# Kernel tuning notes

Measured on AMD Instinct MI355X. Metric: run time of the kernel, lower is better.

The kernel has to match this reference:

```python
import math
import jax, jax.numpy as jnp
import numpy as np

B, T, D_MODEL, H = 8, 2048, 1024, 16
D_HEAD = D_MODEL // H


def _rel_shift(x):
    # x: (B, T, H, H) -- faithful port of the TF pad/reshape/slice trick,
    # which in this module operates on the time axis (dim 1).
    b, t, h, h2 = x.shape
    x = jnp.pad(x, ((0, 0), (1, 0), (0, 0), (0, 0)))  # (B, T+1, H, H)
    x = x.reshape(t + 1, b, h, h2)[1:]                 # drop first row
    return x.reshape(b, t, h, h2)


def setup_inputs() -> dict:
    key = jax.random.key(0)
    ks = jax.random.split(key, 16)
    s = 1.0 / math.sqrt(D_MODEL)
    return {
        "inputs": jax.random.normal(ks[0], (B, T, D_MODEL), jnp.float32),
        "pos_embedding": jax.random.normal(ks[1], (B, T, D_MODEL), jnp.float32),
        "masks": jnp.ones((B, T), dtype=bool),
        "Wq": jax.random.normal(ks[2], (D_MODEL, D_MODEL), jnp.float32) * s,
        "bq": jnp.zeros((D_MODEL,), jnp.float32),
        "Wk": jax.random.normal(ks[3], (D_MODEL, D_MODEL), jnp.float32) * s,
        "bk": jnp.zeros((D_MODEL,), jnp.float32),
        "Wv": jax.random.normal(ks[4], (D_MODEL, D_MODEL), jnp.float32) * s,
        "bv": jnp.zeros((D_MODEL,), jnp.float32),
        "Wp": jax.random.normal(ks[5], (D_MODEL, D_MODEL), jnp.float32) * s,
        "Wo": jax.random.normal(ks[6], (D_MODEL, D_MODEL), jnp.float32) * s,
        "bo": jnp.zeros((D_MODEL,), jnp.float32),
        "u_bias": jax.random.normal(ks[7], (H, D_HEAD), jnp.float32) * 0.05,
        "v_bias": jax.random.normal(ks[8], (H, D_HEAD), jnp.float32) * 0.05,
    }


def reference(inputs, pos_embedding, masks, Wq, bq, Wk, bk, Wv, bv, Wp, Wo, bo, u_bias, v_bias):
    b, t, _ = inputs.shape
    sqrt_dim = math.sqrt(D_MODEL)
    q = (inputs @ Wq + bq).reshape(b, t, H, D_HEAD)
    k = (inputs @ Wk + bk).reshape(b, t, H, D_HEAD)
    v = (inputs @ Wv + bv).reshape(b, t, H, D_HEAD)
    p = (pos_embedding @ Wp).reshape(b, t, H, D_HEAD)

    # NOTE: no (B,H,T,D) transpose in the original -> HxH scores per timestep.
    content_score = jnp.einsum("bthd,btkd->bthk", q + u_bias, k)  # (B,T,H,H)
    pos_score = jnp.einsum("bthd,btkd->bthk", q + v_bias, p)      # (B,T,H,H)
    pos_score = _rel_shift(pos_score)
    score = (content_score + pos_score) / sqrt_dim
    score = jnp.where(masks[:, :, None, None], score, jnp.float32(1e-9))
    attn = jax.nn.softmax(score, axis=-1)
    ctx = jnp.einsum("bthk,btkd->bthd", attn, v)                  # (B,T,H,D)
    ctx = ctx.transpose(0, 2, 1, 3).reshape(b, -1, D_MODEL)       # (B,T,d_model)
    return ctx @ Wo + bo
```

## Files before the change

kernel.cpp:

```cpp
#include <hip/hip_runtime.h>


typedef __attribute__((ext_vector_type(8))) short short8;
typedef __attribute__((ext_vector_type(4))) float f32x4;

__device__ __forceinline__ ushort f2bf(float f) {
    unsigned u = __float_as_uint(f);
    u += 0x7FFFu + ((u >> 16) & 1u);
    return (ushort)(u >> 16);
}
__device__ __forceinline__ float bf2f(ushort u) {
    return __uint_as_float(((unsigned)u) << 16);
}

typedef const unsigned int __attribute__((address_space(1)))* gas_t;
typedef unsigned int __attribute__((address_space(3)))* las_t;
__device__ __forceinline__ void gl_lds16(const ushort* g, ushort* l) {
    __builtin_amdgcn_global_load_lds((gas_t)g, (las_t)l, 16, 0, 0);
}

__global__ __launch_bounds__(256)
void conv_bf16_k(const float* __restrict__ in, ushort* __restrict__ out)
{
    const size_t i = ((size_t)blockIdx.x * 256 + threadIdx.x) * 8;
    float4 a = *(const float4*)(in + i);
    float4 b = *(const float4*)(in + i + 4);
    short8 o = {(short)f2bf(a.x), (short)f2bf(a.y), (short)f2bf(a.z), (short)f2bf(a.w),
                (short)f2bf(b.x), (short)f2bf(b.y), (short)f2bf(b.z), (short)f2bf(b.w)};
    *(short8*)(out + i) = o;
}

__global__ __launch_bounds__(256)
void transpose5_k(const float* __restrict__ W0, const float* __restrict__ W1,
                  const float* __restrict__ W2, const float* __restrict__ W3,
                  const float* __restrict__ W4, ushort* __restrict__ Wt)
{
    __shared__ float tile[32][33];
    const int z = blockIdx.z;
    const float* W = (z == 0) ? W0 : (z == 1) ? W1 : (z == 2) ? W2 : (z == 3) ? W3 : W4;
    ushort* dst = Wt + (size_t)z * 1024 * 1024;
    const int tx = threadIdx.x & 31;
    const int ty = threadIdx.x >> 5;
    const int n0 = blockIdx.x * 32;
    const int k0 = blockIdx.y * 32;
#pragma unroll
    for (int i = 0; i < 4; ++i)
        tile[ty + i * 8][tx] = W[(size_t)(k0 + ty + i * 8) * 1024 + n0 + tx];
    __syncthreads();
#pragma unroll
    for (int i = 0; i < 4; ++i)
        dst[(size_t)(n0 + ty + i * 8) * 1024 + k0 + tx] = f2bf(tile[tx][ty + i * 8]);
}

__global__ __launch_bounds__(256)
void bias_concat_k(const float* __restrict__ b0, const float* __restrict__ b1,
                   const float* __restrict__ b2, float* __restrict__ out)
{
    const int i = blockIdx.x * 256 + threadIdx.x;
    const int s = i >> 10;
    const int j = i & 1023;
    out[i] = (s == 0) ? b0[j] : (s == 1) ? b1[j] : b2[j];
}


#define VMC(n) asm volatile("s_waitcnt vmcnt(" #n ")" ::: "memory")
#define KDIM 1024

template<int HAS_BIAS, int OUT_BF16>
__global__ __launch_bounds__(512, 4)
void gemm7_k(const ushort* __restrict__ A, const ushort* __restrict__ Bt,
             const float* __restrict__ bias, void* __restrict__ Cv,
             int N)
{
    __shared__ ushort As[3 * 4096];
    __shared__ ushort Bs[3 * 8192];
    const int tid = threadIdx.x;
    const int l = tid & 63;
    const int w = tid >> 6;
    const int wr = w >> 2;
    const int wc = w & 3;

    const int gx = gridDim.x;
    const int lin = blockIdx.y * gx + blockIdx.x;
    const int xcd = lin & 7;
    const int idx = lin >> 3;
    const int hb = gridDim.y >> 3;
    const int sxc = gx >> 2;
    const int g4 = idx >> 4;
    const int li = idx & 15;
    const int bx = (g4 % sxc) * 4 + (li & 3);
    const int by = xcd * hb + (g4 / sxc) * 4 + (li >> 2);
    const int bm = by * 128;
    const int bn = bx * 256;

    const int srow = tid >> 2;
    const int scol = ((tid & 3) ^ ((tid >> 3) & 3)) * 8;
    const ushort* Ag  = A  + (size_t)(bm + srow) * KDIM + scol;
    const ushort* Bg  = Bt + (size_t)(bn + srow) * KDIM + scol;
    const ushort* Bg2 = Bg + (size_t)128 * KDIM;
    const int lw = w * 512;

    const int lr = l & 15;
    const int fb = (((l >> 4) ^ ((l >> 1) & 3)) * 8);
    const int laneA = (wr * 64 + lr) * 32 + fb;
    const int laneB = (wc * 64 + lr) * 32 + fb;

    f32x4 acc[4][4];
#pragma unroll
    for (int i = 0; i < 4; ++i)
#pragma unroll
        for (int n = 0; n < 4; ++n)
            acc[i][n] = (f32x4){0.f, 0.f, 0.f, 0.f};

#define STAGE7(tt, rg) do { \
    ushort* ha = As + (rg) * 4096 + lw; \
    ushort* hbp = Bs + (rg) * 8192 + lw; \
    const size_t ko = (size_t)(tt) * 32; \
    gl_lds16(Ag + ko, ha); \
    gl_lds16(Bg + ko, hbp); \
    gl_lds16(Bg2 + ko, hbp + 4096); \
} while (0)

    STAGE7(0, 0);
    STAGE7(1, 1);
    VMC(3);
    __builtin_amdgcn_s_barrier();
    __builtin_amdgcn_sched_barrier(0);

#pragma unroll
    for (int t = 0; t < 32; ++t) {
        const int cur = t % 3;
        const int stg = (t + 2) % 3;
        if (t + 2 < 32) STAGE7(t + 2, stg);
        const ushort* ap = As + cur * 4096 + laneA;
        const ushort* bp = Bs + cur * 8192 + laneB;
        short8 af[4], bf4[4];
#pragma unroll
        for (int m = 0; m < 4; ++m) af[m] = *(const short8*)(ap + m * 512);
#pragma unroll
        for (int n = 0; n < 4; ++n) bf4[n] = *(const short8*)(bp + n * 512);
        if (t < 30) { VMC(3); }
        else if (t == 30) { VMC(0); }
        asm volatile("s_waitcnt lgkmcnt(0)" ::: "memory");
        __builtin_amdgcn_s_barrier();
        __builtin_amdgcn_sched_barrier(0);
#pragma unroll
        for (int m = 0; m < 4; ++m)
#pragma unroll
            for (int n = 0; n < 4; ++n)
                acc[m][n] = __builtin_amdgcn_mfma_f32_16x16x32_bf16(af[m], bf4[n], acc[m][n], 0, 0, 0);
    }
#undef STAGE7

    const int cr = (l >> 4) * 4;
    const int cc = l & 15;
    float bv[4];
#pragma unroll
    for (int n = 0; n < 4; ++n)
        bv[n] = HAS_BIAS ? bias[bn + wc * 64 + n * 16 + cc] : 0.f;
#pragma unroll
    for (int m = 0; m < 4; ++m) {
#pragma unroll
        for (int n = 0; n < 4; ++n) {
            const int col = bn + wc * 64 + n * 16 + cc;
#pragma unroll
            for (int r = 0; r < 4; ++r) {
                const int row = bm + wr * 64 + m * 16 + cr + r;
                float v = acc[m][n][r] + bv[n];
                if (OUT_BF16) ((ushort*)Cv)[(size_t)row * N + col] = f2bf(v);
                else          ((float*)Cv)[(size_t)row * N + col] = v;
            }
        }
    }
}

__global__ __launch_bounds__(256)
void attn2_k(const ushort* __restrict__ qkv, const ushort* __restrict__ pbuf,
             const float* __restrict__ ubias, const float* __restrict__ vbias,
             const int* __restrict__ masks, ushort* __restrict__ ctx)
{
    __shared__ __align__(16) float Pl[4][16 * 20];

    const int tid = threadIdx.x;
    const int w = tid >> 6;
    const int l = tid & 63;
    const int m = blockIdx.x * 4 + w;
    const int b2 = m >> 11;
    const int t2 = m & 2047;
    const int f  = m + 8;
    const int bs = f / 2049;
    const int ts = f - bs * 2049;
    const bool haspos = (ts != 0);
    const int mp = bs * 2048 + ts - 1;

    const int lr = l & 15;
    const int g  = l >> 4;
    const int ko = g * 8;

    const ushort* qb = qkv + (size_t)m * 3072;

    short8 quf[2], kf[2], qvf[2], pf[2];
#pragma unroll
    for (int c = 0; c < 2; ++c) {
        const int off = lr * 64 + c * 32 + ko;
        short8 q = *(const short8*)(qb + off);
        kf[c]    = *(const short8*)(qb + 1024 + off);
        float4 u0 = *(const float4*)(ubias + off);
        float4 u1 = *(const float4*)(ubias + off + 4);
        quf[c] = (short8){
            (short)f2bf(bf2f((ushort)q[0]) + u0.x), (short)f2bf(bf2f((ushort)q[1]) + u0.y),
            (short)f2bf(bf2f((ushort)q[2]) + u0.z), (short)f2bf(bf2f((ushort)q[3]) + u0.w),
            (short)f2bf(bf2f((ushort)q[4]) + u1.x), (short)f2bf(bf2f((ushort)q[5]) + u1.y),
            (short)f2bf(bf2f((ushort)q[6]) + u1.z), (short)f2bf(bf2f((ushort)q[7]) + u1.w)};
    }
    if (haspos) {
        const ushort* qmp = qkv + (size_t)mp * 3072;
        const ushort* pp  = pbuf + (size_t)mp * 1024;
#pragma unroll
        for (int c = 0; c < 2; ++c) {
            const int off = lr * 64 + c * 32 + ko;
            short8 q = *(const short8*)(qmp + off);
            pf[c]    = *(const short8*)(pp + off);
            float4 v0 = *(const float4*)(vbias + off);
            float4 v1 = *(const float4*)(vbias + off + 4);
            qvf[c] = (short8){
                (short)f2bf(bf2f((ushort)q[0]) + v0.x), (short)f2bf(bf2f((ushort)q[1]) + v0.y),
                (short)f2bf(bf2f((ushort)q[2]) + v0.z), (short)f2bf(bf2f((ushort)q[3]) + v0.w),
                (short)f2bf(bf2f((ushort)q[4]) + v1.x), (short)f2bf(bf2f((ushort)q[5]) + v1.y),
                (short)f2bf(bf2f((ushort)q[6]) + v1.z), (short)f2bf(bf2f((ushort)q[7]) + v1.w)};
        }
    }

    f32x4 s = (f32x4){0.f, 0.f, 0.f, 0.f};
    s = __builtin_amdgcn_mfma_f32_16x16x32_bf16(quf[0], kf[0], s, 0, 0, 0);
    s = __builtin_amdgcn_mfma_f32_16x16x32_bf16(quf[1], kf[1], s, 0, 0, 0);
    if (haspos) {
        s = __builtin_amdgcn_mfma_f32_16x16x32_bf16(qvf[0], pf[0], s, 0, 0, 0);
        s = __builtin_amdgcn_mfma_f32_16x16x32_bf16(qvf[1], pf[1], s, 0, 0, 0);
    }

    const bool mk = (masks[m] != 0);
    float sc[4];
#pragma unroll
    for (int r = 0; r < 4; ++r)
        sc[r] = mk ? s[r] * 0.03125f : 1e-9f;

    float mx[4], ex[4], sm[4];
#pragma unroll
    for (int r = 0; r < 4; ++r) {
        mx[r] = sc[r];
#pragma unroll
        for (int o = 8; o; o >>= 1) mx[r] = fmaxf(mx[r], __shfl_xor(mx[r], o, 64));
        ex[r] = __expf(sc[r] - mx[r]);
        sm[r] = ex[r];
#pragma unroll
        for (int o = 8; o; o >>= 1) sm[r] += __shfl_xor(sm[r], o, 64);
    }

    float* pw = Pl[w];
#pragma unroll
    for (int r = 0; r < 4; ++r)
        pw[(g * 4 + r) * 20 + lr] = ex[r] / sm[r];

    short8 pa;
    if (g < 2) {
        float4 p0 = *(const float4*)(pw + lr * 20 + g * 8);
        float4 p1 = *(const float4*)(pw + lr * 20 + g * 8 + 4);
        pa = (short8){(short)f2bf(p0.x), (short)f2bf(p0.y), (short)f2bf(p0.z), (short)f2bf(p0.w),
                      (short)f2bf(p1.x), (short)f2bf(p1.y), (short)f2bf(p1.z), (short)f2bf(p1.w)};
    } else {
        pa = (short8){0, 0, 0, 0, 0, 0, 0, 0};
    }

    const ushort* vb0 = qb + 2048;
    const size_t orow_base = (size_t)b2 * 2048 + (t2 >> 4);
    const int ocol_base = (t2 & 15) * 64;
#pragma unroll
    for (int n = 0; n < 4; ++n) {
        const int d0 = n * 16;
        short8 vf;
        if (g < 2) {
#pragma unroll
            for (int j = 0; j < 8; ++j)
                vf[j] = (short)vb0[(ko + j) * 64 + d0 + lr];
        } else {
            vf = (short8){0, 0, 0, 0, 0, 0, 0, 0};
        }
        f32x4 o = (f32x4){0.f, 0.f, 0.f, 0.f};
        o = __builtin_amdgcn_mfma_f32_16x16x32_bf16(pa, vf, o, 0, 0, 0);
#pragma unroll
        for (int r = 0; r < 4; ++r) {
            const int h1 = g * 4 + r;
            ctx[(orow_base + (size_t)h1 * 128) * 1024 + ocol_base + d0 + lr] = f2bf(o[r]);
        }
    }
}

extern "C" void kernel_launch(void* const* d_in, const int* in_sizes, int n_in,
                              void* d_out, int out_size, void* d_ws, size_t ws_size,
                              hipStream_t stream)
{
    (void)in_sizes; (void)n_in; (void)out_size; (void)ws_size;
    const float* inputs = (const float*)d_in[0];
    const float* pos    = (const float*)d_in[1];
    const int*   masks  = (const int*)d_in[2];
    const float* Wq = (const float*)d_in[3];
    const float* bq = (const float*)d_in[4];
    const float* Wk = (const float*)d_in[5];
    const float* bk = (const float*)d_in[6];
    const float* Wv = (const float*)d_in[7];
    const float* bv = (const float*)d_in[8];
    const float* Wp = (const float*)d_in[9];
    const float* Wo = (const float*)d_in[10];
    const float* bo = (const float*)d_in[11];
    const float* ub = (const float*)d_in[12];
    const float* vb = (const float*)d_in[13];

    char* ws = (char*)d_ws;
    const size_t WT_SZ = (size_t)1024 * 1024 * 2;
    ushort* WT  = (ushort*)(ws);
    ushort* WqT = WT;
    ushort* WpT = (ushort*)(ws + 3 * WT_SZ);
    ushort* WoT = (ushort*)(ws + 4 * WT_SZ);
    float*  biascat = (float*)(ws + 5 * WT_SZ);
    char* bufs = ws + 5 * WT_SZ + 65536;
    const size_t S_SZ = (size_t)16384 * 1024 * 2;
    ushort* S1 = (ushort*)(bufs);
    ushort* S2 = (ushort*)(bufs + S_SZ);
    ushort* S3 = (ushort*)(bufs + 2 * S_SZ);

    dim3 blk(256);

    transpose5_k<<<dim3(32, 32, 5), blk, 0, stream>>>(Wq, Wk, Wv, Wp, Wo, WT);
    bias_concat_k<<<dim3(12), blk, 0, stream>>>(bq, bk, bv, biascat);

    conv_bf16_k<<<dim3(8192), blk, 0, stream>>>(pos, S1);
    gemm7_k<0, 1><<<dim3(4, 128), dim3(512), 0, stream>>>(S1, WpT, nullptr, S2, 1024);

    conv_bf16_k<<<dim3(8192), blk, 0, stream>>>(inputs, S1);
    gemm7_k<1, 1><<<dim3(12, 128), dim3(512), 0, stream>>>(S1, WqT, biascat, S3, 3072);

    attn2_k<<<dim3(4096), blk, 0, stream>>>(S3, S2, ub, vb, masks, S1);

    gemm7_k<1, 0><<<dim3(4, 128), dim3(512), 0, stream>>>(S1, WoT, bo, (float*)d_out, 1024);
}
```

Baseline: 274.7 us.

## Software-pipeline MFMA with LDS fragment loads in bf16 GEMM

```diff
diff --git a/kernel.cpp b/kernel.cpp
--- a/kernel.cpp
+++ b/kernel.cpp
@@ -67,8 +67,8 @@
 #define KDIM 1024
 
 template<int HAS_BIAS, int OUT_BF16>
-__global__ __launch_bounds__(512, 4)
-void gemm7_k(const ushort* __restrict__ A, const ushort* __restrict__ Bt,
+__global__ __launch_bounds__(512, 2)
+void gemm9_k(const ushort* __restrict__ A, const ushort* __restrict__ Bt,
              const float* __restrict__ bias, void* __restrict__ Cv,
              int N)
 {
@@ -112,7 +112,9 @@
         for (int n = 0; n < 4; ++n)
             acc[i][n] = (f32x4){0.f, 0.f, 0.f, 0.f};
 
-#define STAGE7(tt, rg) do { \
+    short8 fa[2][4], fbv[2][4];
+
+#define STAGE9(tt, rg) do { \
     ushort* ha = As + (rg) * 4096 + lw; \
     ushort* hbp = Bs + (rg) * 8192 + lw; \
     const size_t ko = (size_t)(tt) * 32; \
@@ -121,8 +123,8 @@
     gl_lds16(Bg2 + ko, hbp + 4096); \
 } while (0)
 
-    STAGE7(0, 0);
-    STAGE7(1, 1);
+    STAGE9(0, 0);
+    STAGE9(1, 1);
     VMC(3);
     __builtin_amdgcn_s_barrier();
     __builtin_amdgcn_sched_barrier(0);
@@ -131,26 +133,34 @@
     for (int t = 0; t < 32; ++t) {
         const int cur = t % 3;
         const int stg = (t + 2) % 3;
-        if (t + 2 < 32) STAGE7(t + 2, stg);
+        const int pb = t & 1;
+        if (t + 2 < 32) STAGE9(t + 2, stg);
         const ushort* ap = As + cur * 4096 + laneA;
         const ushort* bp = Bs + cur * 8192 + laneB;
-        short8 af[4], bf4[4];
-#pragma unroll
-        for (int m = 0; m < 4; ++m) af[m] = *(const short8*)(ap + m * 512);
-#pragma unroll
-        for (int n = 0; n < 4; ++n) bf4[n] = *(const short8*)(bp + n * 512);
+#pragma unroll
+        for (int m = 0; m < 4; ++m) fa[pb][m] = *(const short8*)(ap + m * 512);
+#pragma unroll
+        for (int n = 0; n < 4; ++n) fbv[pb][n] = *(const short8*)(bp + n * 512);
+        if (t > 0) {
+            const int qb2 = (t - 1) & 1;
+#pragma unroll
+            for (int m = 0; m < 4; ++m)
+#pragma unroll
+                for (int n = 0; n < 4; ++n)
+                    acc[m][n] = __builtin_amdgcn_mfma_f32_16x16x32_bf16(fa[qb2][m], fbv[qb2][n], acc[m][n], 0, 0, 0);
+        }
         if (t < 30) { VMC(3); }
         else if (t == 30) { VMC(0); }
         asm volatile("s_waitcnt lgkmcnt(0)" ::: "memory");
         __builtin_amdgcn_s_barrier();
         __builtin_amdgcn_sched_barrier(0);
-#pragma unroll
-        for (int m = 0; m < 4; ++m)
-#pragma unroll
-            for (int n = 0; n < 4; ++n)
-                acc[m][n] = __builtin_amdgcn_mfma_f32_16x16x32_bf16(af[m], bf4[n], acc[m][n], 0, 0, 0);
-    }
-#undef STAGE7
+    }
+#pragma unroll
+    for (int m = 0; m < 4; ++m)
+#pragma unroll
+        for (int n = 0; n < 4; ++n)
+            acc[m][n] = __builtin_amdgcn_mfma_f32_16x16x32_bf16(fa[1][m], fbv[1][n], acc[m][n], 0, 0, 0);
+#undef STAGE9
 
     const int cr = (l >> 4) * 4;
     const int cc = l & 15;
@@ -335,12 +345,12 @@
     bias_concat_k<<<dim3(12), blk, 0, stream>>>(bq, bk, bv, biascat);
 
     conv_bf16_k<<<dim3(8192), blk, 0, stream>>>(pos, S1);
-    gemm7_k<0, 1><<<dim3(4, 128), dim3(512), 0, stream>>>(S1, WpT, nullptr, S2, 1024);
+    gemm9_k<0, 1><<<dim3(4, 128), dim3(512), 0, stream>>>(S1, WpT, nullptr, S2, 1024);
 
     conv_bf16_k<<<dim3(8192), blk, 0, stream>>>(inputs, S1);
-    gemm7_k<1, 1><<<dim3(12, 128), dim3(512), 0, stream>>>(S1, WqT, biascat, S3, 3072);
+    gemm9_k<1, 1><<<dim3(12, 128), dim3(512), 0, stream>>>(S1, WqT, biascat, S3, 3072);
 
     attn2_k<<<dim3(4096), blk, 0, stream>>>(S3, S2, ub, vb, masks, S1);
 
-    gemm7_k<1, 0><<<dim3(4, 128), dim3(512), 0, stream>>>(S1, WoT, bo, (float*)d_out, 1024);
-}
+    gemm9_k<1, 0><<<dim3(4, 128), dim3(512), 0, stream>>>(S1, WoT, bo, (float*)d_out, 1024);
+}
```

Result: no change. 275.4 us (median of 2 runs) (+0.3%).
